# Performance work log

Measured on AMD Instinct MI355X. Metric: run time of the kernel, lower is better.

The kernel has to match this reference:

```python
import jax, jax.numpy as jnp
import numpy as np

B, T, V, E, H, FC, O = 4096, 64, 512, 32, 128, 256, 1024


def setup_inputs() -> dict:
    key = jax.random.key(0)
    ks = jax.random.split(key, 12)
    n = lambda k, shape, sc=1.0: (jax.random.normal(k, shape, jnp.float32) * sc)
    return {
        "message": n(ks[0], (B, T, V), 0.1),
        "W_emb": n(ks[1], (E, V), 0.05),
        "b_emb": n(ks[2], (E,), 0.05),
        "init_emb": n(ks[3], (1, 1, E), 1.0),
        "W_ih": n(ks[4], (3 * H, E), 0.08),
        "W_hh": n(ks[5], (3 * H, H), 0.08),
        "b_ih": n(ks[6], (3 * H,), 0.05),
        "b_hh": n(ks[7], (3 * H,), 0.05),
        "W_fc1": n(ks[8], (FC, H), 0.08),
        "b_fc1": n(ks[9], (FC,), 0.05),
        "W_fc2": n(ks[10], (O, FC), 0.05),
        "b_fc2": n(ks[11], (O,), 0.05),
    }


def reference(message, W_emb, b_emb, init_emb, W_ih, W_hh, b_ih, b_hh,
              W_fc1, b_fc1, W_fc2, b_fc2):
    Bb, Tt, Vv = message.shape
    Hh = W_hh.shape[1]
    # Per-step embedding of the message (torch does this inside the loop;
    # it is a pure per-timestep linear so we batch it once): [B,T,E]
    emb = jnp.einsum('btv,ev->bte', message, W_emb) + b_emb
    # Inputs consumed by the GRU at step t: initial_embedding at t=0,
    # then embedding(message[:, t-1]) for t >= 1. The embedding of the
    # final token is computed in torch but never fed to the GRU.
    x0 = jnp.broadcast_to(init_emb[0], (Bb, init_emb.shape[-1]))  # [B,E]
    xs = jnp.concatenate([x0[:, None, :], emb[:, :Tt - 1, :]], axis=1)  # [B,T,E]
    # Precompute input-side gate pre-activations for all steps: [T,B,3H]
    gi_all = jnp.einsum('bte,ge->tbg', xs, W_ih) + b_ih

    def gru_step(h, gi):
        gh = h @ W_hh.T + b_hh  # [B,3H]
        i_r, i_z, i_n = jnp.split(gi, 3, axis=-1)
        h_r, h_z, h_n = jnp.split(gh, 3, axis=-1)
        r = jax.nn.sigmoid(i_r + h_r)
        z = jax.nn.sigmoid(i_z + h_z)
        nng = jnp.tanh(i_n + r * h_n)
        h_new = (1.0 - z) * nng + z * h
        return h_new, None

    h0 = jnp.zeros((Bb, Hh), message.dtype)
    h_last, _ = jax.lax.scan(gru_step, h0, gi_all)
    hid = jax.nn.elu(h_last @ W_fc1.T + b_fc1)
    return jax.nn.sigmoid(hid @ W_fc2.T + b_fc2)
```

## Files before the change

### kernel.cpp

```cpp
#include <hip/hip_runtime.h>
#include <math.h>

#define B_ 4096
#define T_ 64
#define V_ 512
#define E_ 32
#define H_ 128
#define FC1_ 256
#define O_ 1024

typedef float f32x4 __attribute__((ext_vector_type(4)));
typedef short s16x8 __attribute__((ext_vector_type(8)));
typedef unsigned short u16;

#define MFMA16(a, b, c) __builtin_amdgcn_mfma_f32_16x16x32_bf16(a, b, c, 0, 0, 0)

#define LDS_BARRIER() do {                                   \
    asm volatile("s_waitcnt lgkmcnt(0)" ::: "memory");       \
    __builtin_amdgcn_s_barrier();                            \
} while (0)

union Frag { u16 q[8]; s16x8 v; };

__device__ __forceinline__ u16 f2bf(float f) {
    union { float f; unsigned u; } v; v.f = f;
    unsigned r = v.u + 0x7FFFu + ((v.u >> 16) & 1u);
    return (u16)(r >> 16);
}
__device__ __forceinline__ float sigf(float x) { return 1.0f / (1.0f + __expf(-x)); }
__device__ __forceinline__ float tanhfast(float x) {
    return 1.0f - 2.0f / (__expf(2.0f * x) + 1.0f);
}

__global__ void __launch_bounds__(256) prep_kernel(
    const float* __restrict__ Wih, const float* __restrict__ Whh,
    const float* __restrict__ Wemb, const float* __restrict__ Wfc1,
    const float* __restrict__ Wfc2,
    u16* __restrict__ wihF, u16* __restrict__ whhF, u16* __restrict__ wembF,
    u16* __restrict__ wfc1F, u16* __restrict__ wfc2F) {
    int id = blockIdx.x * 256 + threadIdx.x;
    int np = gridDim.x * 256;
    for (int i = id; i < 24 * 4 * 64 * 8; i += np) {
        int j = i & 7, l = (i >> 3) & 63, kc = (i >> 9) & 3, gt = i >> 11;
        whhF[i] = f2bf(Whh[(gt * 16 + (l & 15)) * 128 + kc * 32 + (l >> 4) * 8 + j]);
    }
    for (int i = id; i < 24 * 64 * 8; i += np) {
        int j = i & 7, l = (i >> 3) & 63, gt = i >> 9;
        wihF[i] = f2bf(Wih[(gt * 16 + (l & 15)) * 32 + (l >> 4) * 8 + j]);
    }
    for (int i = id; i < 2 * 16 * 64 * 8; i += np) {
        int j = i & 7, l = (i >> 3) & 63, kc = (i >> 9) & 15, nt = i >> 13;
        wembF[i] = f2bf(Wemb[(nt * 16 + (l & 15)) * 512 + kc * 32 + (l >> 4) * 8 + j]);
    }
    for (int i = id; i < 16 * 4 * 64 * 8; i += np) {
        int j = i & 7, l = (i >> 3) & 63, kc = (i >> 9) & 3, ot = i >> 11;
        wfc1F[i] = f2bf(Wfc1[(ot * 16 + (l & 15)) * 128 + kc * 32 + (l >> 4) * 8 + j]);
    }
    for (int i = id; i < 64 * 8 * 64 * 8; i += np) {
        int j = i & 7, l = (i >> 3) & 63, kc = (i >> 9) & 7, nt = i >> 12;
        wfc2F[i] = f2bf(Wfc2[(nt * 16 + (l & 15)) * 256 + kc * 32 + (l >> 4) * 8 + j]);
    }
}

__global__ void __launch_bounds__(256, 1) fused_kernel(
    const float* __restrict__ msg,
    const u16* __restrict__ whhF8, const u16* __restrict__ wihF8,
    const u16* __restrict__ wembF8,
    const float* __restrict__ b_ih, const float* __restrict__ b_hh,
    const float* __restrict__ b_emb, const float* __restrict__ init_emb,
    const u16* __restrict__ wfc1F8, const float* __restrict__ b_fc1,
    const u16* __restrict__ wfc2F8, const float* __restrict__ b_fc2,
    float* __restrict__ out) {
    __shared__ u16 hlds[2][16 * 136];
    __shared__ float epart[4][512];
    __shared__ u16 xfrag[16 * 40];
    __shared__ u16 hidl[16 * 264];
    const int tid = threadIdx.x, w = tid >> 6, l = tid & 63;
    const int ln = l & 15, lh = l >> 4;
    const int gb = blockIdx.x;

    for (int i = tid; i < 16 * 136; i += 256) hlds[0][i] = 0;

    const s16x8* whhFv = (const s16x8*)whhF8;
    const s16x8* wihFv = (const s16x8*)wihF8;
    const s16x8* wembFv = (const s16x8*)wembF8;
    s16x8 wh[2][3][4], wi[2][3], we0[4], we1[4];
    float br[2], bz[2], bin[2], bgn[2];
    #pragma unroll
    for (int p = 0; p < 2; p++) {
        #pragma unroll
        for (int g = 0; g < 3; g++) {
            int gt = w + 4 * p + 8 * g;
            #pragma unroll
            for (int kc = 0; kc < 4; kc++) wh[p][g][kc] = whhFv[(gt * 4 + kc) * 64 + l];
            wi[p][g] = wihFv[gt * 64 + l];
        }
        int c = w * 16 + p * 64 + ln;
        br[p]  = b_ih[c] + b_hh[c];
        bz[p]  = b_ih[128 + c] + b_hh[128 + c];
        bin[p] = b_ih[256 + c];
        bgn[p] = b_hh[256 + c];
    }
    #pragma unroll
    for (int kc = 0; kc < 4; kc++) {
        we0[kc] = wembFv[(4 * w + kc) * 64 + l];
        we1[kc] = wembFv[(16 + 4 * w + kc) * 64 + l];
    }
    const float bev = b_emb[tid & 31];

    s16x8 xcur;
    {
        Frag xi;
        #pragma unroll
        for (int j = 0; j < 8; j++) xi.q[j] = f2bf(init_emb[lh * 8 + j]);
        xcur = xi.v;
    }
    float hold[2][4] = {};
    const float* mrow = msg + ((size_t)(gb * 16 + ln) * 64) * 512 + (4 * w) * 32 + lh * 8;
    f32x4 mA[8], mB[8];
    #pragma unroll
    for (int kc = 0; kc < 4; kc++) {
        mA[2 * kc]     = *(const f32x4*)(mrow + kc * 32);
        mA[2 * kc + 1] = *(const f32x4*)(mrow + kc * 32 + 4);
    }
    LDS_BARRIER();

    const int aoff = ln * 136 + lh * 8;

#define GRU_STEP(T, MC, MN) do {                                               \
    const int t = (T);                                                         \
    const u16* hb = hlds[t & 1];                                               \
    s16x8 af0 = *(const s16x8*)(hb + aoff);                                    \
    s16x8 af1 = *(const s16x8*)(hb + aoff + 32);                               \
    s16x8 af2 = *(const s16x8*)(hb + aoff + 64);                               \
    s16x8 af3 = *(const s16x8*)(hb + aoff + 96);                               \
    if (t < 62) {                                                              \
        const float* p_ = mrow + (size_t)(t + 1) * 512;                        \
        _Pragma("unroll")                                                      \
        for (int kc = 0; kc < 4; kc++) {                                       \
            MN[2 * kc]     = *(const f32x4*)(p_ + kc * 32);                    \
            MN[2 * kc + 1] = *(const f32x4*)(p_ + kc * 32 + 4);                \
        }                                                                      \
    }                                                                          \
    f32x4 ar[2], az[2], agn[2], ain[2];                                        \
    _Pragma("unroll")                                                          \
    for (int p = 0; p < 2; p++) {                                              \
        ar[p]  = {br[p], br[p], br[p], br[p]};                                 \
        az[p]  = {bz[p], bz[p], bz[p], bz[p]};                                 \
        agn[p] = {bgn[p], bgn[p], bgn[p], bgn[p]};                             \
        ain[p] = {bin[p], bin[p], bin[p], bin[p]};                             \
    }                                                                          \
    _Pragma("unroll")                                                          \
    for (int p = 0; p < 2; p++) {                                              \
        ar[p]  = MFMA16(af0, wh[p][0][0], ar[p]);                              \
        ar[p]  = MFMA16(af1, wh[p][0][1], ar[p]);                              \
        ar[p]  = MFMA16(af2, wh[p][0][2], ar[p]);                              \
        ar[p]  = MFMA16(af3, wh[p][0][3], ar[p]);                              \
        az[p]  = MFMA16(af0, wh[p][1][0], az[p]);                              \
        az[p]  = MFMA16(af1, wh[p][1][1], az[p]);                              \
        az[p]  = MFMA16(af2, wh[p][1][2], az[p]);                              \
        az[p]  = MFMA16(af3, wh[p][1][3], az[p]);                              \
        agn[p] = MFMA16(af0, wh[p][2][0], agn[p]);                             \
        agn[p] = MFMA16(af1, wh[p][2][1], agn[p]);                             \
        agn[p] = MFMA16(af2, wh[p][2][2], agn[p]);                             \
        agn[p] = MFMA16(af3, wh[p][2][3], agn[p]);                             \
        ar[p]  = MFMA16(xcur, wi[p][0], ar[p]);                                \
        az[p]  = MFMA16(xcur, wi[p][1], az[p]);                                \
        ain[p] = MFMA16(xcur, wi[p][2], ain[p]);                               \
    }                                                                          \
    u16* hw = hlds[(t + 1) & 1];                                               \
    _Pragma("unroll")                                                          \
    for (int p = 0; p < 2; p++) {                                              \
        int colo = w * 16 + p * 64 + ln;                                       \
        _Pragma("unroll")                                                      \
        for (int i = 0; i < 4; i++) {                                          \
            float rg = sigf(ar[p][i]);                                         \
            float zg = sigf(az[p][i]);                                         \
            float ng = tanhfast(ain[p][i] + rg * agn[p][i]);                   \
            float hn = zg * (hold[p][i] - ng) + ng;                            \
            hold[p][i] = hn;                                                   \
            hw[(lh * 4 + i) * 136 + colo] = f2bf(hn);                          \
        }                                                                      \
    }                                                                          \
    if (t < 63) {                                                              \
        f32x4 e0 = {0.f, 0.f, 0.f, 0.f}, e1 = {0.f, 0.f, 0.f, 0.f};            \
        _Pragma("unroll")                                                      \
        for (int kc = 0; kc < 4; kc++) {                                       \
            Frag fa;                                                           \
            _Pragma("unroll")                                                  \
            for (int j = 0; j < 4; j++) {                                      \
                fa.q[j]     = f2bf(MC[2 * kc][j]);                             \
                fa.q[4 + j] = f2bf(MC[2 * kc + 1][j]);                         \
            }                                                                  \
            e0 = MFMA16(fa.v, we0[kc], e0);                                    \
            e1 = MFMA16(fa.v, we1[kc], e1);                                    \
        }                                                                      \
        _Pragma("unroll")                                                      \
        for (int i = 0; i < 4; i++) {                                          \
            epart[w][(lh * 4 + i) * 32 + ln]      = e0[i];                     \
            epart[w][(lh * 4 + i) * 32 + 16 + ln] = e1[i];                     \
        }                                                                      \
    }                                                                          \
    LDS_BARRIER();                                                             \
    if (t < 63) {                                                              \
        _Pragma("unroll")                                                      \
        for (int u = 0; u < 2; u++) {                                          \
            int f = tid + 256 * u;                                             \
            float s = epart[0][f] + epart[1][f] + epart[2][f] + epart[3][f]    \
                      + bev;                                                   \
            xfrag[(f >> 5) * 40 + (f & 31)] = f2bf(s);                         \
        }                                                                      \
        LDS_BARRIER();                                                         \
        xcur = *(const s16x8*)(xfrag + ln * 40 + lh * 8);                      \
    }                                                                          \
} while (0)

    for (int tt = 0; tt < 64; tt += 2) {
        GRU_STEP(tt, mA, mB);
        GRU_STEP(tt + 1, mB, mA);
    }
#undef GRU_STEP

    const u16* hb = hlds[0];
    s16x8 hf0 = *(const s16x8*)(hb + aoff);
    s16x8 hf1 = *(const s16x8*)(hb + aoff + 32);
    s16x8 hf2 = *(const s16x8*)(hb + aoff + 64);
    s16x8 hf3 = *(const s16x8*)(hb + aoff + 96);
    const s16x8* w1v = (const s16x8*)wfc1F8;
    #pragma unroll
    for (int q = 0; q < 4; q++) {
        int ot = w * 4 + q;
        float b1 = b_fc1[ot * 16 + ln];
        f32x4 a1 = {b1, b1, b1, b1};
        a1 = MFMA16(hf0, w1v[(ot * 4 + 0) * 64 + l], a1);
        a1 = MFMA16(hf1, w1v[(ot * 4 + 1) * 64 + l], a1);
        a1 = MFMA16(hf2, w1v[(ot * 4 + 2) * 64 + l], a1);
        a1 = MFMA16(hf3, w1v[(ot * 4 + 3) * 64 + l], a1);
        #pragma unroll
        for (int i = 0; i < 4; i++) {
            float v = a1[i];
            v = v > 0.0f ? v : (__expf(v) - 1.0f);
            hidl[(lh * 4 + i) * 264 + ot * 16 + ln] = f2bf(v);
        }
    }
    __syncthreads();

    s16x8 hf[8];
    #pragma unroll
    for (int kc = 0; kc < 8; kc++)
        hf[kc] = *(const s16x8*)(hidl + ln * 264 + kc * 32 + lh * 8);
    const s16x8* w2v = (const s16x8*)wfc2F8;
    #pragma unroll
    for (int q = 0; q < 16; q++) {
        int nt = w * 16 + q;
        float b2 = b_fc2[nt * 16 + ln];
        f32x4 a2 = {b2, b2, b2, b2};
        #pragma unroll
        for (int kc = 0; kc < 8; kc++)
            a2 = MFMA16(hf[kc], w2v[(nt * 8 + kc) * 64 + l], a2);
        #pragma unroll
        for (int i = 0; i < 4; i++)
            out[(size_t)(gb * 16 + lh * 4 + i) * 1024 + nt * 16 + ln] = sigf(a2[i]);
    }
}

extern "C" void kernel_launch(void* const* d_in, const int* in_sizes, int n_in,
                              void* d_out, int out_size, void* d_ws, size_t ws_size,
                              hipStream_t stream) {
    const float* message  = (const float*)d_in[0];
    const float* W_emb    = (const float*)d_in[1];
    const float* b_emb    = (const float*)d_in[2];
    const float* init_emb = (const float*)d_in[3];
    const float* W_ih     = (const float*)d_in[4];
    const float* W_hh     = (const float*)d_in[5];
    const float* b_ih     = (const float*)d_in[6];
    const float* b_hh     = (const float*)d_in[7];
    const float* W_fc1    = (const float*)d_in[8];
    const float* b_fc1    = (const float*)d_in[9];
    const float* W_fc2    = (const float*)d_in[10];
    const float* b_fc2    = (const float*)d_in[11];
    float* out = (float*)d_out;

    u16* whhF  = (u16*)d_ws;
    u16* wihF  = whhF  + 49152;
    u16* wembF = wihF  + 12288;
    u16* wfc1F = wembF + 16384;
    u16* wfc2F = wfc1F + 32768;

    hipLaunchKernelGGL(prep_kernel, dim3(256), dim3(256), 0, stream,
                       W_ih, W_hh, W_emb, W_fc1, W_fc2, wihF, whhF, wembF, wfc1F, wfc2F);
    hipLaunchKernelGGL(fused_kernel, dim3(256), dim3(256), 0, stream,
                       message, whhF, wihF, wembF, b_ih, b_hh, b_emb, init_emb,
                       wfc1F, b_fc1, wfc2F, b_fc2, out);
}
```

Baseline: 150.4 us.

## Double waves per block to 512 threads and deepen message prefetch to three steps

Each block now runs 8 waves instead of 4, so each wave owns one gate column tile instead of two. The embedding K-split is spread over 8 partial sums and the FC work is split twice as finely. The message prefetch now uses a 4-buffer rotation that loads three timesteps ahead instead of one. The aim is to shorten the per-step serial critical path of the recurrence and hide global memory latency better. The cost is more barrier participants and an 8-way LDS reduction each step, with the grid still at 256 blocks.

```diff
diff --git a/kernel.cpp b/kernel.cpp
--- a/kernel.cpp
+++ b/kernel.cpp
@@ -62,7 +62,7 @@
     }
 }
 
-__global__ void __launch_bounds__(256, 1) fused_kernel(
+__global__ void __launch_bounds__(512, 2) fused_kernel(
     const float* __restrict__ msg,
     const u16* __restrict__ whhF8, const u16* __restrict__ wihF8,
     const u16* __restrict__ wembF8,
@@ -72,39 +72,39 @@
     const u16* __restrict__ wfc2F8, const float* __restrict__ b_fc2,
     float* __restrict__ out) {
     __shared__ u16 hlds[2][16 * 136];
-    __shared__ float epart[4][512];
+    __shared__ float epart[8][16 * 36];
     __shared__ u16 xfrag[16 * 40];
     __shared__ u16 hidl[16 * 264];
     const int tid = threadIdx.x, w = tid >> 6, l = tid & 63;
     const int ln = l & 15, lh = l >> 4;
+    const int wg = w & 3, wp = w >> 2;
     const int gb = blockIdx.x;
 
-    for (int i = tid; i < 16 * 136; i += 256) hlds[0][i] = 0;
+    for (int i = tid; i < 16 * 136; i += 512) hlds[0][i] = 0;
 
     const s16x8* whhFv = (const s16x8*)whhF8;
     const s16x8* wihFv = (const s16x8*)wihF8;
     const s16x8* wembFv = (const s16x8*)wembF8;
-    s16x8 wh[2][3][4], wi[2][3], we0[4], we1[4];
-    float br[2], bz[2], bin[2], bgn[2];
-    #pragma unroll
-    for (int p = 0; p < 2; p++) {
+    s16x8 wh[3][4], wi[3], we[2][2];
+    float br, bz, bin, bgn;
+    {
         #pragma unroll
         for (int g = 0; g < 3; g++) {
-            int gt = w + 4 * p + 8 * g;
+            int gt = wg + 4 * wp + 8 * g;
             #pragma unroll
-            for (int kc = 0; kc < 4; kc++) wh[p][g][kc] = whhFv[(gt * 4 + kc) * 64 + l];
-            wi[p][g] = wihFv[gt * 64 + l];
+            for (int kc = 0; kc < 4; kc++) wh[g][kc] = whhFv[(gt * 4 + kc) * 64 + l];
+            wi[g] = wihFv[gt * 64 + l];
         }
-        int c = w * 16 + p * 64 + ln;
-        br[p]  = b_ih[c] + b_hh[c];
-        bz[p]  = b_ih[128 + c] + b_hh[128 + c];
-        bin[p] = b_ih[256 + c];
-        bgn[p] = b_hh[256 + c];
-    }
-    #pragma unroll
-    for (int kc = 0; kc < 4; kc++) {
-        we0[kc] = wembFv[(4 * w + kc) * 64 + l];
-        we1[kc] = wembFv[(16 + 4 * w + kc) * 64 + l];
+        int c = wg * 16 + wp * 64 + ln;
+        br  = b_ih[c] + b_hh[c];
+        bz  = b_ih[128 + c] + b_hh[128 + c];
+        bin = b_ih[256 + c];
+        bgn = b_hh[256 + c];
+        #pragma unroll
+        for (int kk = 0; kk < 2; kk++) {
+            we[kk][0] = wembFv[(2 * w + kk) * 64 + l];
+            we[kk][1] = wembFv[(16 + 2 * w + kk) * 64 + l];
+        }
     }
     const float bev = b_emb[tid & 31];
 
@@ -115,111 +115,98 @@
         for (int j = 0; j < 8; j++) xi.q[j] = f2bf(init_emb[lh * 8 + j]);
         xcur = xi.v;
     }
-    float hold[2][4] = {};
-    const float* mrow = msg + ((size_t)(gb * 16 + ln) * 64) * 512 + (4 * w) * 32 + lh * 8;
-    f32x4 mA[8], mB[8];
-    #pragma unroll
-    for (int kc = 0; kc < 4; kc++) {
-        mA[2 * kc]     = *(const f32x4*)(mrow + kc * 32);
-        mA[2 * kc + 1] = *(const f32x4*)(mrow + kc * 32 + 4);
-    }
+    float hold[4] = {};
+    const float* mrow = msg + (size_t)(gb * 16 + ln) * T_ * V_ + (2 * w) * 32 + lh * 8;
+    f32x4 mb0[4], mb1[4], mb2[4], mb3[4];
+#define LOADCOL(BUF, C) do {                                   \
+    const float* p_ = mrow + (size_t)(C) * 512;                \
+    BUF[0] = *(const f32x4*)(p_);                              \
+    BUF[1] = *(const f32x4*)(p_ + 4);                          \
+    BUF[2] = *(const f32x4*)(p_ + 32);                         \
+    BUF[3] = *(const f32x4*)(p_ + 36);                         \
+} while (0)
+    LOADCOL(mb0, 0); LOADCOL(mb1, 1); LOADCOL(mb2, 2);
     LDS_BARRIER();
 
     const int aoff = ln * 136 + lh * 8;
+    const int colo = wg * 16 + wp * 64 + ln;
 
 #define GRU_STEP(T, MC, MN) do {                                               \
     const int t = (T);                                                         \
+    if (t <= 59) LOADCOL(MN, t + 3);                                           \
     const u16* hb = hlds[t & 1];                                               \
     s16x8 af0 = *(const s16x8*)(hb + aoff);                                    \
     s16x8 af1 = *(const s16x8*)(hb + aoff + 32);                               \
     s16x8 af2 = *(const s16x8*)(hb + aoff + 64);                               \
     s16x8 af3 = *(const s16x8*)(hb + aoff + 96);                               \
-    if (t < 62) {                                                              \
-        const float* p_ = mrow + (size_t)(t + 1) * 512;                        \
-        _Pragma("unroll")                                                      \
-        for (int kc = 0; kc < 4; kc++) {                                       \
-            MN[2 * kc]     = *(const f32x4*)(p_ + kc * 32);                    \
-            MN[2 * kc + 1] = *(const f32x4*)(p_ + kc * 32 + 4);                \
-        }                                                                      \
-    }                                                                          \
-    f32x4 ar[2], az[2], agn[2], ain[2];                                        \
-    _Pragma("unroll")                                                          \
-    for (int p = 0; p < 2; p++) {                                              \
-        ar[p]  = {br[p], br[p], br[p], br[p]};                                 \
-        az[p]  = {bz[p], bz[p], bz[p], bz[p]};                                 \
-        agn[p] = {bgn[p], bgn[p], bgn[p], bgn[p]};                             \
-        ain[p] = {bin[p], bin[p], bin[p], bin[p]};                             \
-    }                                                                          \
-    _Pragma("unroll")                                                          \
-    for (int p = 0; p < 2; p++) {                                              \
-        ar[p]  = MFMA16(af0, wh[p][0][0], ar[p]);                              \
-        ar[p]  = MFMA16(af1, wh[p][0][1], ar[p]);                              \
-        ar[p]  = MFMA16(af2, wh[p][0][2], ar[p]);                              \
-        ar[p]  = MFMA16(af3, wh[p][0][3], ar[p]);                              \
-        az[p]  = MFMA16(af0, wh[p][1][0], az[p]);                              \
-        az[p]  = MFMA16(af1, wh[p][1][1], az[p]);                              \
-        az[p]  = MFMA16(af2, wh[p][1][2], az[p]);                              \
-        az[p]  = MFMA16(af3, wh[p][1][3], az[p]);                              \
-        agn[p] = MFMA16(af0, wh[p][2][0], agn[p]);                             \
-        agn[p] = MFMA16(af1, wh[p][2][1], agn[p]);                             \
-        agn[p] = MFMA16(af2, wh[p][2][2], agn[p]);                             \
-        agn[p] = MFMA16(af3, wh[p][2][3], agn[p]);                             \
-        ar[p]  = MFMA16(xcur, wi[p][0], ar[p]);                                \
-        az[p]  = MFMA16(xcur, wi[p][1], az[p]);                                \
-        ain[p] = MFMA16(xcur, wi[p][2], ain[p]);                               \
-    }                                                                          \
+    f32x4 ar  = {br, br, br, br};                                              \
+    f32x4 az  = {bz, bz, bz, bz};                                              \
+    f32x4 agn = {bgn, bgn, bgn, bgn};                                          \
+    f32x4 ain = {bin, bin, bin, bin};                                          \
+    ar  = MFMA16(xcur, wi[0], ar);                                             \
+    az  = MFMA16(xcur, wi[1], az);                                             \
+    ain = MFMA16(xcur, wi[2], ain);                                            \
+    ar  = MFMA16(af0, wh[0][0], ar);                                           \
+    ar  = MFMA16(af1, wh[0][1], ar);                                           \
+    ar  = MFMA16(af2, wh[0][2], ar);                                           \
+    ar  = MFMA16(af3, wh[0][3], ar);                                           \
+    az  = MFMA16(af0, wh[1][0], az);                                           \
+    az  = MFMA16(af1, wh[1][1], az);                                           \
+    az  = MFMA16(af2, wh[1][2], az);                                           \
+    az  = MFMA16(af3, wh[1][3], az);                                           \
+    agn = MFMA16(af0, wh[2][0], agn);                                          \
+    agn = MFMA16(af1, wh[2][1], agn);                                          \
+    agn = MFMA16(af2, wh[2][2], agn);                                          \
+    agn = MFMA16(af3, wh[2][3], agn);                                          \
     u16* hw = hlds[(t + 1) & 1];                                               \
     _Pragma("unroll")                                                          \
-    for (int p = 0; p < 2; p++) {                                              \
-        int colo = w * 16 + p * 64 + ln;                                       \
-        _Pragma("unroll")                                                      \
-        for (int i = 0; i < 4; i++) {                                          \
-            float rg = sigf(ar[p][i]);                                         \
-            float zg = sigf(az[p][i]);                                         \
-            float ng = tanhfast(ain[p][i] + rg * agn[p][i]);                   \
-            float hn = zg * (hold[p][i] - ng) + ng;                            \
-            hold[p][i] = hn;                                                   \
-            hw[(lh * 4 + i) * 136 + colo] = f2bf(hn);                          \
-        }                                                                      \
+    for (int i = 0; i < 4; i++) {                                              \
+        float rg = sigf(ar[i]);                                                \
+        float zg = sigf(az[i]);                                                \
+        float ng = tanhfast(ain[i] + rg * agn[i]);                             \
+        float hn = zg * (hold[i] - ng) + ng;                                   \
+        hold[i] = hn;                                                          \
+        hw[(lh * 4 + i) * 136 + colo] = f2bf(hn);                              \
     }                                                                          \
     if (t < 63) {                                                              \
         f32x4 e0 = {0.f, 0.f, 0.f, 0.f}, e1 = {0.f, 0.f, 0.f, 0.f};            \
         _Pragma("unroll")                                                      \
-        for (int kc = 0; kc < 4; kc++) {                                       \
+        for (int kk = 0; kk < 2; kk++) {                                       \
             Frag fa;                                                           \
             _Pragma("unroll")                                                  \
             for (int j = 0; j < 4; j++) {                                      \
-                fa.q[j]     = f2bf(MC[2 * kc][j]);                             \
-                fa.q[4 + j] = f2bf(MC[2 * kc + 1][j]);                         \
+                fa.q[j]     = f2bf(MC[2 * kk][j]);                             \
+                fa.q[4 + j] = f2bf(MC[2 * kk + 1][j]);                         \
             }                                                                  \
-            e0 = MFMA16(fa.v, we0[kc], e0);                                    \
-            e1 = MFMA16(fa.v, we1[kc], e1);                                    \
+            e0 = MFMA16(fa.v, we[kk][0], e0);                                  \
+            e1 = MFMA16(fa.v, we[kk][1], e1);                                  \
         }                                                                      \
         _Pragma("unroll")                                                      \
         for (int i = 0; i < 4; i++) {                                          \
-            epart[w][(lh * 4 + i) * 32 + ln]      = e0[i];                     \
-            epart[w][(lh * 4 + i) * 32 + 16 + ln] = e1[i];                     \
+            epart[w][(lh * 4 + i) * 36 + ln]      = e0[i];                     \
+            epart[w][(lh * 4 + i) * 36 + 16 + ln] = e1[i];                     \
         }                                                                      \
     }                                                                          \
     LDS_BARRIER();                                                             \
     if (t < 63) {                                                              \
-        _Pragma("unroll")                                                      \
-        for (int u = 0; u < 2; u++) {                                          \
-            int f = tid + 256 * u;                                             \
-            float s = epart[0][f] + epart[1][f] + epart[2][f] + epart[3][f]    \
-                      + bev;                                                   \
-            xfrag[(f >> 5) * 40 + (f & 31)] = f2bf(s);                         \
-        }                                                                      \
+        int fr = tid >> 5, fc = tid & 31, fo = fr * 36 + fc;                   \
+        float s = epart[0][fo] + epart[1][fo] + epart[2][fo] + epart[3][fo]    \
+                + epart[4][fo] + epart[5][fo] + epart[6][fo] + epart[7][fo]    \
+                + bev;                                                         \
+        xfrag[fr * 40 + fc] = f2bf(s);                                         \
         LDS_BARRIER();                                                         \
         xcur = *(const s16x8*)(xfrag + ln * 40 + lh * 8);                      \
     }                                                                          \
 } while (0)
 
-    for (int tt = 0; tt < 64; tt += 2) {
-        GRU_STEP(tt, mA, mB);
-        GRU_STEP(tt + 1, mB, mA);
+    for (int tt = 0; tt < 64; tt += 4) {
+        GRU_STEP(tt + 0, mb0, mb3);
+        GRU_STEP(tt + 1, mb1, mb0);
+        GRU_STEP(tt + 2, mb2, mb1);
+        GRU_STEP(tt + 3, mb3, mb2);
     }
 #undef GRU_STEP
+#undef LOADCOL
 
     const u16* hb = hlds[0];
     s16x8 hf0 = *(const s16x8*)(hb + aoff);
@@ -228,8 +215,8 @@
     s16x8 hf3 = *(const s16x8*)(hb + aoff + 96);
     const s16x8* w1v = (const s16x8*)wfc1F8;
     #pragma unroll
-    for (int q = 0; q < 4; q++) {
-        int ot = w * 4 + q;
+    for (int q = 0; q < 2; q++) {
+        int ot = 2 * w + q;
         float b1 = b_fc1[ot * 16 + ln];
         f32x4 a1 = {b1, b1, b1, b1};
         a1 = MFMA16(hf0, w1v[(ot * 4 + 0) * 64 + l], a1);
@@ -243,7 +230,7 @@
             hidl[(lh * 4 + i) * 264 + ot * 16 + ln] = f2bf(v);
         }
     }
-    __syncthreads();
+    LDS_BARRIER();
 
     s16x8 hf[8];
     #pragma unroll
@@ -251,8 +238,8 @@
         hf[kc] = *(const s16x8*)(hidl + ln * 264 + kc * 32 + lh * 8);
     const s16x8* w2v = (const s16x8*)wfc2F8;
     #pragma unroll
-    for (int q = 0; q < 16; q++) {
-        int nt = w * 16 + q;
+    for (int q = 0; q < 8; q++) {
+        int nt = 8 * w + q;
         float b2 = b_fc2[nt * 16 + ln];
         f32x4 a2 = {b2, b2, b2, b2};
         #pragma unroll
@@ -289,7 +276,7 @@
 
     hipLaunchKernelGGL(prep_kernel, dim3(256), dim3(256), 0, stream,
                        W_ih, W_hh, W_emb, W_fc1, W_fc2, wihF, whhF, wembF, wfc1F, wfc2F);
-    hipLaunchKernelGGL(fused_kernel, dim3(256), dim3(256), 0, stream,
+    hipLaunchKernelGGL(fused_kernel, dim3(256), dim3(512), 0, stream,
                        message, whhF, wihF, wembF, b_ih, b_hh, b_emb, init_emb,
                        wfc1F, b_fc1, wfc2F, b_fc2, out);
 }
```

Result: faster. 138.1 us (-8.2%).
